# Optimization experiments

Hardware: AMD Instinct MI355X
Metric: run time of the kernel (lower is better)

Reference implementation:

```python
import jax, jax.numpy as jnp
import numpy as np

B, T, N, K, DEG = 4, 256, 4096, 64, 4
L = T - 1                # number of transition steps
NNZ = B * N * DEG        # COO entries per step


def setup_inputs() -> dict:
    key = jax.random.key(0)
    k1, k2, k3, k4, k5 = jax.random.split(key, 5)
    observation = jax.random.normal(k1, (B, T, K), dtype=jnp.float32)
    W_em = jax.random.normal(k2, (K, N), dtype=jnp.float32) * 0.05
    duration = jax.random.randint(k3, (B,), 1, T + 1)  # in [1, T]
    # COO layout: for each batch b and each source state s, DEG outgoing edges
    src = jnp.tile(jnp.repeat(jnp.arange(N, dtype=jnp.int32), DEG), (B,))   # [NNZ]
    bidx = jnp.repeat(jnp.arange(B, dtype=jnp.int32), N * DEG)              # [NNZ]
    tgt = jax.random.randint(k4, (L, NNZ), 0, N, dtype=jnp.int32)
    # guarantee a self-loop so every target state has >=1 incoming edge
    self_mask = (jnp.arange(NNZ) % DEG) == 0
    tgt = jnp.where(self_mask[None, :], src[None, :], tgt)
    trans_idx = jnp.stack([jnp.broadcast_to(bidx, (L, NNZ)),
                           jnp.broadcast_to(src, (L, NNZ)),
                           tgt], axis=-1)                                   # [L,NNZ,3]
    trans_logvals = jnp.log(jax.random.uniform(k5, (L, NNZ), minval=0.1, maxval=1.0,
                                               dtype=jnp.float32))
    return {"observation": observation, "W_em": W_em, "duration": duration,
            "trans_idx": trans_idx, "trans_logvals": trans_logvals}


def _forward_alpha(observation, W_em, trans_idx, trans_logvals):
    # emission log-probs [B,T,N]
    em = jax.nn.log_softmax(jnp.einsum('btk,kn->btn', observation, W_em), axis=-1)
    la0 = em[:, 0, :] - jnp.log(jnp.float32(N))  # uniform start distribution

    def step(la_prev, inp):
        idx, lv, e = inp  # idx [NNZ,3], lv [NNZ], e [B,N]
        b, s, t = idx[:, 0], idx[:, 1], idx[:, 2]
        seg = b * N + t
        contrib = la_prev[b, s] + lv  # log_alpha[b,src] + log A[b,src,tgt]
        # numerically-stable segmented logsumexp over incoming edges per (b,tgt)
        m = jax.ops.segment_max(contrib, seg, num_segments=B * N)
        m_safe = jnp.where(jnp.isfinite(m), m, 0.0)
        ssum = jax.ops.segment_sum(jnp.exp(contrib - m_safe[seg]), seg,
                                   num_segments=B * N)
        ssum_safe = jnp.where(ssum > 0, ssum, 1.0)
        la = jnp.where(ssum > 0, jnp.log(ssum_safe) + m_safe, -jnp.inf)
        la = la.reshape(B, N) + e
        return la, la

    em_t = jnp.swapaxes(em, 0, 1)  # [T,B,N]
    _, las = jax.lax.scan(step, la0, (trans_idx, trans_logvals, em_t[1:]))
    log_alpha = jnp.concatenate([la0[None], las], axis=0)  # [T,B,N]
    return jnp.swapaxes(log_alpha, 0, 1)  # [B,T,N]


def reference(observation, W_em, duration, trans_idx, trans_logvals):
    log_alpha = _forward_alpha(observation, W_em, trans_idx, trans_logvals)
    log_sums = jax.nn.logsumexp(log_alpha, axis=2)                # [B,T]
    log_probs = jnp.take_along_axis(log_sums, duration[:, None] - 1, axis=1)  # [B,1]
    return log_probs
```

## Files before the change

kernel.cpp:

```cpp
#include <hip/hip_runtime.h>
#include <hip/hip_bf16.h>


#define Bc 4
#define Tc 256
#define Nc 4096
#define Kc 64
#define DEGc 4
#define Lc (Tc - 1)
#define NNZc (Bc * Nc * DEGc)
#define NPB 8
#define TPB 512
#define TPB_EM 256
#define NODES_PER (Nc / NPB)
#define LOG_N 8.31776616671934f

__device__ __forceinline__ float cohLoadF(const float* p) {
  return __hip_atomic_load((float*)p, __ATOMIC_RELAXED, __HIP_MEMORY_SCOPE_AGENT);
}
__device__ __forceinline__ void cohStoreF(float* p, float v) {
  __hip_atomic_store(p, v, __ATOMIC_RELAXED, __HIP_MEMORY_SCOPE_AGENT);
}

template <int NT>
__device__ __forceinline__ float blockSumT(float v, volatile float* red) {
#pragma unroll
  for (int o = 1; o < 64; o <<= 1) v += __shfl_xor(v, o, 64);
  __syncthreads();
  if ((threadIdx.x & 63) == 0) red[threadIdx.x >> 6] = v;
  __syncthreads();
  float s = 0.f;
#pragma unroll
  for (int k = 0; k < NT / 64; ++k) s += red[k];
  return s;
}
template <int NT>
__device__ __forceinline__ float blockMaxT(float v, volatile float* red) {
#pragma unroll
  for (int o = 1; o < 64; o <<= 1) v = fmaxf(v, __shfl_xor(v, o, 64));
  __syncthreads();
  if ((threadIdx.x & 63) == 0) red[threadIdx.x >> 6] = v;
  __syncthreads();
  float m = -INFINITY;
#pragma unroll
  for (int k = 0; k < NT / 64; ++k) m = fmaxf(m, red[k]);
  return m;
}

__global__ __launch_bounds__(TPB_EM) void em_kernel(const float* __restrict__ obs,
                                                    const float* __restrict__ W,
                                                    float* __restrict__ em) {
  const int r = blockIdx.x, tid = threadIdx.x;
  __shared__ float o[Kc];
  __shared__ float red[8];
  if (tid < Kc) o[tid] = obs[(size_t)r * Kc + tid];
  __syncthreads();
  float4 acc[4];
#pragma unroll
  for (int gI = 0; gI < 4; ++gI) acc[gI] = make_float4(0.f, 0.f, 0.f, 0.f);
  const float4* W4 = (const float4*)W;
  for (int k = 0; k < Kc; ++k) {
    const float ov = o[k];
    const float4* wr = W4 + (size_t)k * (Nc / 4);
#pragma unroll
    for (int gI = 0; gI < 4; ++gI) {
      float4 w = wr[gI * 256 + tid];
      acc[gI].x = fmaf(ov, w.x, acc[gI].x);
      acc[gI].y = fmaf(ov, w.y, acc[gI].y);
      acc[gI].z = fmaf(ov, w.z, acc[gI].z);
      acc[gI].w = fmaf(ov, w.w, acc[gI].w);
    }
  }
  float m = -INFINITY;
#pragma unroll
  for (int gI = 0; gI < 4; ++gI)
    m = fmaxf(m, fmaxf(fmaxf(acc[gI].x, acc[gI].y), fmaxf(acc[gI].z, acc[gI].w)));
  m = blockMaxT<TPB_EM>(m, red);
  float s = 0.f;
#pragma unroll
  for (int gI = 0; gI < 4; ++gI)
    s += __expf(acc[gI].x - m) + __expf(acc[gI].y - m) + __expf(acc[gI].z - m) + __expf(acc[gI].w - m);
  s = blockSumT<TPB_EM>(s, red);
  const float lse = m + __logf(s);
  float4* em4 = (float4*)em;
#pragma unroll
  for (int gI = 0; gI < 4; ++gI) {
    float4 w = acc[gI];
    w.x -= lse; w.y -= lse; w.z -= lse; w.w -= lse;
    em4[(size_t)r * (Nc / 4) + gI * 256 + tid] = w;
  }
}

__global__ __launch_bounds__(TPB) void scan_kernel(
    const int* __restrict__ duration,
    const int* __restrict__ tidx,
    const float* __restrict__ tlv,
    const float* __restrict__ em,
    float* __restrict__ part,
    float* __restrict__ Spart,
    unsigned int* __restrict__ cnt,
    float* __restrict__ out) {
  const int g = blockIdx.x;
  const int b = g / NPB, sl = g % NPB;
  const int tid = threadIdx.x;
  __shared__ float red[TPB / 64];
  __shared__ float lsb[Nc];

  const int node = sl * NODES_PER + tid;
  const size_t ebase = (size_t)b * (Nc * DEGc) + (size_t)node * DEGc;
  unsigned int* mycnt = cnt + b * 16;

#pragma unroll
  for (int i = 0; i < Nc / TPB; ++i) lsb[i * TPB + tid] = 0.f;

  float la = em[((size_t)b * Tc) * Nc + node] - LOG_N;
  int4 c0, c1, c2; float4 cl;
  {
    const int4* ip = (const int4*)tidx + ((ebase * 3) >> 2);
    c0 = ip[0]; c1 = ip[1]; c2 = ip[2];
    cl = ((const float4*)tlv)[ebase >> 2];
  }
  int4 n0, n1, n2; float4 nl;
  {
    const size_t e = ebase + (size_t)NNZc;
    const int4* ip = (const int4*)tidx + ((e * 3) >> 2);
    n0 = ip[0]; n1 = ip[1]; n2 = ip[2];
    nl = ((const float4*)tlv)[e >> 2];
  }
  float em_nxt = em[((size_t)b * Tc + 1) * Nc + node];

  {
    float tot = blockSumT<TPB>(__expf(la), red);
    if (tid == 0) cohStoreF(&Spart[(0 * Bc + b) * 16 + sl], tot);
  }

  for (int t = 1; t <= Lc; ++t) {
    atomicAdd(&lsb[c0.z], __expf(la + cl.x));
    atomicAdd(&lsb[c1.y], __expf(la + cl.y));
    atomicAdd(&lsb[c2.x], __expf(la + cl.z));
    atomicAdd(&lsb[c2.w], __expf(la + cl.w));
    __syncthreads();

    float* pp = part + (((size_t)(t & 1) * Bc + b) * NPB + sl) * Nc;
#pragma unroll
    for (int i = 0; i < Nc / TPB; ++i) {
      const int j = i * TPB + tid;
      float pv = lsb[j];
      lsb[j] = 0.f;
      cohStoreF(&pp[j], pv);
    }
    __syncthreads();

    if (tid == 0) {
      __hip_atomic_fetch_add(mycnt, 1u, __ATOMIC_RELAXED, __HIP_MEMORY_SCOPE_AGENT);
      const unsigned target = (unsigned)NPB * (unsigned)t;
      while (__hip_atomic_load(mycnt, __ATOMIC_RELAXED, __HIP_MEMORY_SCOPE_AGENT) < target)
        __builtin_amdgcn_s_sleep(1);
    }
    __syncthreads();

    const float* pbase = part + ((size_t)(t & 1) * Bc + b) * NPB * Nc;
    float pk[NPB];
#pragma unroll
    for (int k = 0; k < NPB; ++k) pk[k] = cohLoadF(&pbase[(size_t)k * Nc + node]);
    float Sprev = 0.f;
#pragma unroll
    for (int k = 0; k < NPB; ++k) Sprev += cohLoadF(&Spart[((size_t)(t - 1) * Bc + b) * 16 + k]);

    int4 m0 = n0, m1 = n1, m2 = n2; float4 ml = nl;
    if (t <= Lc - 2) {
      const size_t e = (size_t)(t + 1) * NNZc + ebase;
      const int4* ip = (const int4*)tidx + ((e * 3) >> 2);
      m0 = ip[0]; m1 = ip[1]; m2 = ip[2];
      ml = ((const float4*)tlv)[e >> 2];
    }
    float em_fut = em_nxt;
    if (t < Lc) em_fut = em[((size_t)b * Tc + t + 1) * Nc + node];

    float sv = 0.f;
#pragma unroll
    for (int k = 0; k < NPB; ++k) sv += pk[k];
    const float v = __logf(sv) + em_nxt;
    float tot = blockSumT<TPB>(__expf(v), red);
    if (tid == 0) cohStoreF(&Spart[((size_t)t * Bc + b) * 16 + sl], tot);
    la = v - __logf(Sprev);

    c0 = n0; c1 = n1; c2 = n2; cl = nl;
    n0 = m0; n1 = m1; n2 = m2; nl = ml;
    em_nxt = em_fut;
  }

  __syncthreads();
  if (tid == 0) {
    __hip_atomic_fetch_add(mycnt, 1u, __ATOMIC_RELAXED, __HIP_MEMORY_SCOPE_AGENT);
    const unsigned target = (unsigned)NPB * (unsigned)Tc;
    while (__hip_atomic_load(mycnt, __ATOMIC_RELAXED, __HIP_MEMORY_SCOPE_AGENT) < target)
      __builtin_amdgcn_s_sleep(1);
  }
  __syncthreads();

  if (sl == 0) {
    const int tstar = duration[b] - 1;
    float v = 0.0f;
    if (tid < Tc) {
      const int tau = tid;
      if (tau == tstar || tau <= tstar - 2) {
        float Sv = 0.f;
#pragma unroll
        for (int k = 0; k < NPB; ++k) Sv += cohLoadF(&Spart[((size_t)tau * Bc + b) * 16 + k]);
        v = __logf(Sv);
      }
    }
    float tot = blockSumT<TPB>(v, red);
    if (tid == 0) out[b] = tot;
  }
}

extern "C" void kernel_launch(void* const* d_in, const int* in_sizes, int n_in,
                              void* d_out, int out_size, void* d_ws, size_t ws_size,
                              hipStream_t stream) {
  const float* obs = (const float*)d_in[0];
  const float* W = (const float*)d_in[1];
  const int* duration = (const int*)d_in[2];
  const int* tidx = (const int*)d_in[3];
  const float* tlv = (const float*)d_in[4];
  float* out = (float*)d_out;

  float* em = (float*)d_ws;
  float* part = em + (size_t)Bc * Tc * Nc;
  float* Spart = part + (size_t)2 * Bc * NPB * Nc;
  unsigned int* cnt = (unsigned int*)(Spart + (size_t)Tc * Bc * 16);

  hipMemsetAsync(cnt, 0, 64 * sizeof(unsigned int), stream);

  em_kernel<<<dim3(Bc * Tc), dim3(TPB_EM), 0, stream>>>(obs, W, em);
  scan_kernel<<<dim3(Bc * NPB), dim3(TPB), 0, stream>>>(duration, tidx, tlv, em,
                                                        part, Spart, cnt, out);
}
```

Baseline: 1.733 ms.

## Run scan in linear domain with per-block flag barrier and early stop at duration

Stores exponentiated emissions and carries the forward recursion as scaled probabilities, so the per-edge exp of the log-alpha and the per-step log are removed. The shared atomic counter barrier is replaced by per-block 64-bit flag slots that pack the step number with the partial sum, which removes the separate partial-sum array and a barrier round-trip. Partials are written with vectorized coherent stores, and each batch stops looping at its own duration instead of running all steps. The linear-domain rescaling could underflow or overflow differently from the log-domain version, and the inline-asm store and polling add ordering risk.

```diff
diff --git a/kernel.cpp b/kernel.cpp
--- a/kernel.cpp
+++ b/kernel.cpp
@@ -1,6 +1,5 @@
 #include <hip/hip_runtime.h>
 #include <hip/hip_bf16.h>
-
 
 #define Bc 4
 #define Tc 256
@@ -13,13 +12,15 @@
 #define TPB 512
 #define TPB_EM 256
 #define NODES_PER (Nc / NPB)
-#define LOG_N 8.31776616671934f
+#define INV_N (1.0f / 4096.0f)
+
+typedef float f32x4 __attribute__((ext_vector_type(4)));
 
 __device__ __forceinline__ float cohLoadF(const float* p) {
   return __hip_atomic_load((float*)p, __ATOMIC_RELAXED, __HIP_MEMORY_SCOPE_AGENT);
 }
-__device__ __forceinline__ void cohStoreF(float* p, float v) {
-  __hip_atomic_store(p, v, __ATOMIC_RELAXED, __HIP_MEMORY_SCOPE_AGENT);
+__device__ __forceinline__ void cohStore4(float* p, f32x4 v) {
+  asm volatile("global_store_dwordx4 %0, %1, off sc0 sc1" :: "v"(p), "v"(v) : "memory");
 }
 
 template <int NT>
@@ -49,7 +50,7 @@
 
 __global__ __launch_bounds__(TPB_EM) void em_kernel(const float* __restrict__ obs,
                                                     const float* __restrict__ W,
-                                                    float* __restrict__ em) {
+                                                    float* __restrict__ emexp) {
   const int r = blockIdx.x, tid = threadIdx.x;
   __shared__ float o[Kc];
   __shared__ float red[8];
@@ -82,12 +83,37 @@
     s += __expf(acc[gI].x - m) + __expf(acc[gI].y - m) + __expf(acc[gI].z - m) + __expf(acc[gI].w - m);
   s = blockSumT<TPB_EM>(s, red);
   const float lse = m + __logf(s);
-  float4* em4 = (float4*)em;
+  float4* em4 = (float4*)emexp;
 #pragma unroll
   for (int gI = 0; gI < 4; ++gI) {
     float4 w = acc[gI];
-    w.x -= lse; w.y -= lse; w.z -= lse; w.w -= lse;
+    w.x = __expf(w.x - lse); w.y = __expf(w.y - lse);
+    w.z = __expf(w.z - lse); w.w = __expf(w.w - lse);
     em4[(size_t)r * (Nc / 4) + gI * 256 + tid] = w;
+  }
+}
+
+__device__ __forceinline__ void publish(unsigned long long* slot, unsigned t, float sp) {
+  union { float f; unsigned u; } c; c.f = sp;
+  unsigned long long v = ((unsigned long long)c.u << 32) | (unsigned long long)t;
+  __hip_atomic_store(slot, v, __ATOMIC_RELAXED, __HIP_MEMORY_SCOPE_AGENT);
+}
+__device__ __forceinline__ float pollFlags(unsigned long long* fb, int parity, unsigned t) {
+  unsigned long long* base = fb + parity * 8;
+  for (;;) {
+    unsigned long long v[8];
+#pragma unroll
+    for (int k = 0; k < 8; ++k)
+      v[k] = __hip_atomic_load(&base[k], __ATOMIC_RELAXED, __HIP_MEMORY_SCOPE_AGENT);
+    bool ok = true;
+    float s = 0.f;
+#pragma unroll
+    for (int k = 0; k < 8; ++k) {
+      ok &= ((unsigned)(v[k] & 0xffffffffull) >= t);
+      union { unsigned u; float f; } c; c.u = (unsigned)(v[k] >> 32);
+      s += c.f;
+    }
+    if (ok) return s;
   }
 }
 
@@ -95,124 +121,100 @@
     const int* __restrict__ duration,
     const int* __restrict__ tidx,
     const float* __restrict__ tlv,
-    const float* __restrict__ em,
+    const float* __restrict__ emexp,
     float* __restrict__ part,
-    float* __restrict__ Spart,
-    unsigned int* __restrict__ cnt,
+    unsigned long long* __restrict__ flags,
     float* __restrict__ out) {
   const int g = blockIdx.x;
   const int b = g / NPB, sl = g % NPB;
   const int tid = threadIdx.x;
   __shared__ float red[TPB / 64];
   __shared__ float lsb[Nc];
+  __shared__ float sprev_sh;
 
   const int node = sl * NODES_PER + tid;
   const size_t ebase = (size_t)b * (Nc * DEGc) + (size_t)node * DEGc;
-  unsigned int* mycnt = cnt + b * 16;
+  unsigned long long* fb = flags + (size_t)b * 16;
+  const int tstar = duration[b] - 1;
 
 #pragma unroll
   for (int i = 0; i < Nc / TPB; ++i) lsb[i * TPB + tid] = 0.f;
 
-  float la = em[((size_t)b * Tc) * Nc + node] - LOG_N;
-  int4 c0, c1, c2; float4 cl;
+  float v = emexp[((size_t)b * Tc) * Nc + node] * INV_N;
+  float Spart = blockSumT<TPB>(v, red);
+  float inv_sprev = 1.0f;
+  float acc = 0.f;
+
+  int4 c0, c1, c2; float4 cl; float em_cur;
   {
     const int4* ip = (const int4*)tidx + ((ebase * 3) >> 2);
     c0 = ip[0]; c1 = ip[1]; c2 = ip[2];
     cl = ((const float4*)tlv)[ebase >> 2];
-  }
-  int4 n0, n1, n2; float4 nl;
-  {
-    const size_t e = ebase + (size_t)NNZc;
-    const int4* ip = (const int4*)tidx + ((e * 3) >> 2);
-    n0 = ip[0]; n1 = ip[1]; n2 = ip[2];
-    nl = ((const float4*)tlv)[e >> 2];
-  }
-  float em_nxt = em[((size_t)b * Tc + 1) * Nc + node];
-
-  {
-    float tot = blockSumT<TPB>(__expf(la), red);
-    if (tid == 0) cohStoreF(&Spart[(0 * Bc + b) * 16 + sl], tot);
-  }
-
-  for (int t = 1; t <= Lc; ++t) {
-    atomicAdd(&lsb[c0.z], __expf(la + cl.x));
-    atomicAdd(&lsb[c1.y], __expf(la + cl.y));
-    atomicAdd(&lsb[c2.x], __expf(la + cl.z));
-    atomicAdd(&lsb[c2.w], __expf(la + cl.w));
+    em_cur = emexp[((size_t)b * Tc + 1) * Nc + node];
+  }
+
+  for (int t = 1; t <= tstar; ++t) {
+    const float a = v * inv_sprev;
+    atomicAdd(&lsb[c0.z], a * __expf(cl.x));
+    atomicAdd(&lsb[c1.y], a * __expf(cl.y));
+    atomicAdd(&lsb[c2.x], a * __expf(cl.z));
+    atomicAdd(&lsb[c2.w], a * __expf(cl.w));
     __syncthreads();
 
     float* pp = part + (((size_t)(t & 1) * Bc + b) * NPB + sl) * Nc;
-#pragma unroll
-    for (int i = 0; i < Nc / TPB; ++i) {
-      const int j = i * TPB + tid;
-      float pv = lsb[j];
-      lsb[j] = 0.f;
-      cohStoreF(&pp[j], pv);
+    {
+      f32x4 w0 = *(const f32x4*)&lsb[tid * 8];
+      f32x4 w1 = *(const f32x4*)&lsb[tid * 8 + 4];
+      *(f32x4*)&lsb[tid * 8] = (f32x4)0.0f;
+      *(f32x4*)&lsb[tid * 8 + 4] = (f32x4)0.0f;
+      cohStore4(&pp[tid * 8], w0);
+      cohStore4(&pp[tid * 8 + 4], w1);
     }
     __syncthreads();
 
     if (tid == 0) {
-      __hip_atomic_fetch_add(mycnt, 1u, __ATOMIC_RELAXED, __HIP_MEMORY_SCOPE_AGENT);
-      const unsigned target = (unsigned)NPB * (unsigned)t;
-      while (__hip_atomic_load(mycnt, __ATOMIC_RELAXED, __HIP_MEMORY_SCOPE_AGENT) < target)
-        __builtin_amdgcn_s_sleep(1);
-    }
-    __syncthreads();
-
-    const float* pbase = part + ((size_t)(t & 1) * Bc + b) * NPB * Nc;
-    float pk[NPB];
-#pragma unroll
-    for (int k = 0; k < NPB; ++k) pk[k] = cohLoadF(&pbase[(size_t)k * Nc + node]);
-    float Sprev = 0.f;
-#pragma unroll
-    for (int k = 0; k < NPB; ++k) Sprev += cohLoadF(&Spart[((size_t)(t - 1) * Bc + b) * 16 + k]);
-
-    int4 m0 = n0, m1 = n1, m2 = n2; float4 ml = nl;
-    if (t <= Lc - 2) {
-      const size_t e = (size_t)(t + 1) * NNZc + ebase;
+      asm volatile("s_waitcnt vmcnt(0)" ::: "memory");
+      publish(&fb[(t & 1) * 8 + sl], (unsigned)t, Spart);
+    }
+
+    int4 m0 = c0, m1 = c1, m2 = c2; float4 ml = cl; float em_nxt = em_cur;
+    if (t < tstar) {
+      const size_t e = (size_t)t * NNZc + ebase;
       const int4* ip = (const int4*)tidx + ((e * 3) >> 2);
       m0 = ip[0]; m1 = ip[1]; m2 = ip[2];
       ml = ((const float4*)tlv)[e >> 2];
-    }
-    float em_fut = em_nxt;
-    if (t < Lc) em_fut = em[((size_t)b * Tc + t + 1) * Nc + node];
-
+      em_nxt = emexp[((size_t)b * Tc + t + 1) * Nc + node];
+    }
+
+    if (tid == 0) {
+      float sp = pollFlags(fb, t & 1, (unsigned)t);
+      sprev_sh = sp;
+      if (sl == 0 && t <= tstar - 1) acc += __logf(sp);
+    }
+    __syncthreads();
+    const float sprev = sprev_sh;
+
+    const float* pbase = part + ((size_t)(t & 1) * Bc + b) * NPB * Nc;
+    float pk[NPB];
+#pragma unroll
+    for (int k = 0; k < NPB; ++k) pk[k] = cohLoadF(&pbase[(size_t)k * Nc + node]);
     float sv = 0.f;
 #pragma unroll
     for (int k = 0; k < NPB; ++k) sv += pk[k];
-    const float v = __logf(sv) + em_nxt;
-    float tot = blockSumT<TPB>(__expf(v), red);
-    if (tid == 0) cohStoreF(&Spart[((size_t)t * Bc + b) * 16 + sl], tot);
-    la = v - __logf(Sprev);
-
-    c0 = n0; c1 = n1; c2 = n2; cl = nl;
-    n0 = m0; n1 = m1; n2 = m2; nl = ml;
-    em_nxt = em_fut;
+    v = sv * em_cur;
+    Spart = blockSumT<TPB>(v, red);
+    inv_sprev = __frcp_rn(sprev);
+
+    c0 = m0; c1 = m1; c2 = m2; cl = ml; em_cur = em_nxt;
   }
 
   __syncthreads();
   if (tid == 0) {
-    __hip_atomic_fetch_add(mycnt, 1u, __ATOMIC_RELAXED, __HIP_MEMORY_SCOPE_AGENT);
-    const unsigned target = (unsigned)NPB * (unsigned)Tc;
-    while (__hip_atomic_load(mycnt, __ATOMIC_RELAXED, __HIP_MEMORY_SCOPE_AGENT) < target)
-      __builtin_amdgcn_s_sleep(1);
-  }
-  __syncthreads();
-
-  if (sl == 0) {
-    const int tstar = duration[b] - 1;
-    float v = 0.0f;
-    if (tid < Tc) {
-      const int tau = tid;
-      if (tau == tstar || tau <= tstar - 2) {
-        float Sv = 0.f;
-#pragma unroll
-        for (int k = 0; k < NPB; ++k) Sv += cohLoadF(&Spart[((size_t)tau * Bc + b) * 16 + k]);
-        v = __logf(Sv);
-      }
-    }
-    float tot = blockSumT<TPB>(v, red);
-    if (tid == 0) out[b] = tot;
+    publish(&fb[((tstar + 1) & 1) * 8 + sl], (unsigned)(tstar + 1), Spart);
+    if (sl == 0) {
+      float sf = pollFlags(fb, (tstar + 1) & 1, (unsigned)(tstar + 1));
+      out[b] = acc + __logf(sf);
+    }
   }
 }
 
@@ -226,14 +228,13 @@
   const float* tlv = (const float*)d_in[4];
   float* out = (float*)d_out;
 
-  float* em = (float*)d_ws;
-  float* part = em + (size_t)Bc * Tc * Nc;
-  float* Spart = part + (size_t)2 * Bc * NPB * Nc;
-  unsigned int* cnt = (unsigned int*)(Spart + (size_t)Tc * Bc * 16);
-
-  hipMemsetAsync(cnt, 0, 64 * sizeof(unsigned int), stream);
-
-  em_kernel<<<dim3(Bc * Tc), dim3(TPB_EM), 0, stream>>>(obs, W, em);
-  scan_kernel<<<dim3(Bc * NPB), dim3(TPB), 0, stream>>>(duration, tidx, tlv, em,
-                                                        part, Spart, cnt, out);
-}
+  float* emexp = (float*)d_ws;
+  float* part = emexp + (size_t)Bc * Tc * Nc;
+  unsigned long long* flags = (unsigned long long*)(part + (size_t)2 * Bc * NPB * Nc);
+
+  (void)hipMemsetAsync(flags, 0, Bc * 16 * sizeof(unsigned long long), stream);
+
+  em_kernel<<<dim3(Bc * Tc), dim3(TPB_EM), 0, stream>>>(obs, W, emexp);
+  scan_kernel<<<dim3(Bc * NPB), dim3(TPB), 0, stream>>>(duration, tidx, tlv, emexp,
+                                                        part, flags, out);
+}
```

After: 1.775 ms. +2.4%, slower.
